# Optimization experiments

Hardware: AMD Instinct MI355X
Metric: run time of the kernel (lower is better)

## Reference

```python
import jax, jax.numpy as jnp
import numpy as np

N_NODES = 40000
N_EDGES = 640000
D = 128


def setup_inputs() -> dict:
    key = jax.random.key(0)
    ks = jax.random.split(key, 7)
    x = jax.random.normal(ks[0], (N_NODES, D), dtype=jnp.float32)
    edge_index = jax.random.randint(ks[1], (2, N_EDGES), 0, N_NODES, dtype=jnp.int64)
    # uniform in [0.5, 1.5) to avoid division blow-up near zero
    edge_attr = jax.random.uniform(ks[2], (N_EDGES,), dtype=jnp.float32) + 0.5
    s = 1.0 / np.sqrt(D)
    W1 = jax.random.uniform(ks[3], (D, D), dtype=jnp.float32, minval=-s, maxval=s)
    b1 = jax.random.uniform(ks[4], (D,), dtype=jnp.float32, minval=-s, maxval=s)
    W2 = jax.random.uniform(ks[5], (D, D), dtype=jnp.float32, minval=-s, maxval=s)
    b2 = jax.random.uniform(ks[6], (D,), dtype=jnp.float32, minval=-s, maxval=s)
    return {"x": x, "edge_index": edge_index, "edge_attr": edge_attr,
            "W1": W1, "b1": b1, "W2": W2, "b2": b2}


def _layer(x, src, dst, edge_attr, W, b, num_nodes):
    # message: gather source features, divide by per-edge scalar
    msg = x[src] / edge_attr[:, None]                      # [E, D]
    # aggregate: scatter-add into destination nodes
    agg = jax.ops.segment_sum(msg, dst, num_segments=num_nodes)  # [N, D]
    # linear (torch: y = x @ W.T + b) then leaky_relu(0.01)
    y = agg @ W.T + b
    return jnp.where(y >= 0, y, 0.01 * y)


def reference(x, edge_index, edge_attr, W1, b1, W2, b2):
    src, dst = edge_index[0], edge_index[1]
    n = x.shape[0]
    x = jnp.maximum(_layer(x, src, dst, edge_attr, W1, b1, n), 0.0)
    x = jnp.maximum(_layer(x, src, dst, edge_attr, W2, b2, n), 0.0)
    return x
```

## Files before the change

### kernel.cpp

```cpp
#include <hip/hip_runtime.h>

#define D 128
#define CAP 64
typedef unsigned short u16;
typedef unsigned int   u32;

typedef __attribute__((ext_vector_type(8))) short short8;
typedef __attribute__((ext_vector_type(4))) float f32x4;

__device__ __forceinline__ u32 f2bf(float f) {
    u32 u = __float_as_uint(f);
    u += 0x7fffu + ((u >> 16) & 1u);
    return u >> 16;
}
__device__ __forceinline__ float2 bf2x2(u32 u) {
    float2 r;
    r.x = __uint_as_float(u << 16);
    r.y = __uint_as_float(u & 0xffff0000u);
    return r;
}

__global__ __launch_bounds__(256) void prep_kernel(
    const float4* __restrict__ x, uint2* __restrict__ xb,
    const float4* __restrict__ W1, const float4* __restrict__ W2,
    uint2* __restrict__ wb1, uint2* __restrict__ wb2,
    const int* __restrict__ src, const int* __restrict__ dst,
    const float* __restrict__ attr, int* __restrict__ counts,
    u32* __restrict__ combo, int E, int n4, int cvtb)
{
    const int bid = blockIdx.x;
    const int t   = threadIdx.x;

    if (bid < cvtb) {
        int i = bid * 256 + t;
        if (i < n4) {
            float4 v = x[i];
            uint2 o;
            o.x = f2bf(v.x) | (f2bf(v.y) << 16);
            o.y = f2bf(v.z) | (f2bf(v.w) << 16);
            xb[i] = o;
        }
    } else if (bid < cvtb + 32) {
        int i = (bid - cvtb) * 256 + t;
        const float4* in = (i < 4096) ? W1 : W2;
        uint2* out = (i < 4096) ? wb1 : wb2;
        int k = i & 4095;
        float4 v = in[k];
        uint2 o;
        o.x = f2bf(v.x) | (f2bf(v.y) << 16);
        o.y = f2bf(v.z) | (f2bf(v.w) << 16);
        out[k] = o;
    } else {
        long long e0 = (long long)(bid - cvtb - 32) * 1024 + t * 4;
        if (e0 + 3 < E) {
            int4   s4 = *(const int4*)(src + e0);
            int4   d4 = *(const int4*)(dst + e0);
            float4 a4 = *(const float4*)(attr + e0);
            int r0 = atomicAdd(&counts[d4.x], 1);
            int r1 = atomicAdd(&counts[d4.y], 1);
            int r2 = atomicAdd(&counts[d4.z], 1);
            int r3 = atomicAdd(&counts[d4.w], 1);
            if (r0 < CAP) combo[((long long)d4.x << 6) + r0] = (u32)s4.x | (f2bf(1.0f / a4.x) << 16);
            if (r1 < CAP) combo[((long long)d4.y << 6) + r1] = (u32)s4.y | (f2bf(1.0f / a4.y) << 16);
            if (r2 < CAP) combo[((long long)d4.z << 6) + r2] = (u32)s4.z | (f2bf(1.0f / a4.z) << 16);
            if (r3 < CAP) combo[((long long)d4.w << 6) + r3] = (u32)s4.w | (f2bf(1.0f / a4.w) << 16);
        } else {
            for (int q = 0; q < 4; ++q) {
                long long e = e0 + q;
                if (e < E) {
                    int dd = dst[e];
                    int r = atomicAdd(&counts[dd], 1);
                    if (r < CAP)
                        combo[((long long)dd << 6) + r] =
                            (u32)src[e] | (f2bf(1.0f / attr[e]) << 16);
                }
            }
        }
    }
}

__global__ __launch_bounds__(256) void gather_kernel(
    const u16* __restrict__ x, const u32* __restrict__ combo,
    const int* __restrict__ counts, u16* __restrict__ agg, int N)
{
    const int node = (blockIdx.x * 256 + threadIdx.x) >> 6;
    if (node >= N) return;
    const int lane = threadIdx.x & 63;

    const int cnt = min(counts[node], CAP);
    const u32 ce = combo[((long long)node << 6) + lane];

    float2 acc[8];
    #pragma unroll
    for (int q = 0; q < 8; ++q) acc[q] = {0.f, 0.f};

    int j = 0;
    for (; j + 7 < cnt; j += 8) {
        u32 ed[8], rw[8];
        #pragma unroll
        for (int q = 0; q < 8; ++q) ed[q] = __shfl(ce, j + q);
        #pragma unroll
        for (int q = 0; q < 8; ++q)
            rw[q] = *(const u32*)(x + (long long)(ed[q] & 0xffffu) * D + lane * 2);
        #pragma unroll
        for (int q = 0; q < 8; ++q) {
            float f = __uint_as_float(ed[q] & 0xffff0000u);
            float2 v = bf2x2(rw[q]);
            acc[q].x += v.x * f; acc[q].y += v.y * f;
        }
    }
    for (; j + 3 < cnt; j += 4) {
        u32 ed[4], rw[4];
        #pragma unroll
        for (int q = 0; q < 4; ++q) ed[q] = __shfl(ce, j + q);
        #pragma unroll
        for (int q = 0; q < 4; ++q)
            rw[q] = *(const u32*)(x + (long long)(ed[q] & 0xffffu) * D + lane * 2);
        #pragma unroll
        for (int q = 0; q < 4; ++q) {
            float f = __uint_as_float(ed[q] & 0xffff0000u);
            float2 v = bf2x2(rw[q]);
            acc[q].x += v.x * f; acc[q].y += v.y * f;
        }
    }
    for (; j < cnt; ++j) {
        u32 e = __shfl(ce, j);
        u32 r = *(const u32*)(x + (long long)(e & 0xffffu) * D + lane * 2);
        float f = __uint_as_float(e & 0xffff0000u);
        float2 v = bf2x2(r);
        acc[0].x += v.x * f; acc[0].y += v.y * f;
    }

    float s0 = ((acc[0].x + acc[1].x) + (acc[2].x + acc[3].x))
             + ((acc[4].x + acc[5].x) + (acc[6].x + acc[7].x));
    float s1 = ((acc[0].y + acc[1].y) + (acc[2].y + acc[3].y))
             + ((acc[4].y + acc[5].y) + (acc[6].y + acc[7].y));
    u32 o = f2bf(s0) | (f2bf(s1) << 16);
    *(u32*)(agg + (long long)node * D + lane * 2) = o;
}

template <bool OUT_BF16>
__global__ __launch_bounds__(256) void mfma_gemm_kernel(
    const u16* __restrict__ A, const u16* __restrict__ Wb,
    const float* __restrict__ b, void* __restrict__ Yv, int N)
{
    const int wv   = threadIdx.x >> 6;
    const int lane = threadIdx.x & 63;
    const int m0   = (blockIdx.x * 4 + wv) * 16;
    const int mrow = lane & 15;
    const int kq   = lane >> 4;

    const u16* arow = A + (long long)(m0 + mrow) * D + kq * 8;
    short8 afr[4];
    #pragma unroll
    for (int ks = 0; ks < 4; ++ks)
        afr[ks] = *(const short8*)(arow + ks * 32);

    #pragma unroll 1
    for (int j = 0; j < 8; ++j) {
        float bias = b[j * 16 + mrow];
        f32x4 acc = {bias, bias, bias, bias};
        const u16* wrow = Wb + (long long)(j * 16 + mrow) * D + kq * 8;
        #pragma unroll
        for (int ks = 0; ks < 4; ++ks) {
            short8 bfr = *(const short8*)(wrow + ks * 32);
            acc = __builtin_amdgcn_mfma_f32_16x16x32_bf16(afr[ks], bfr, acc, 0, 0, 0);
        }
        #pragma unroll
        for (int r = 0; r < 4; ++r) {
            float v = acc[r] > 0.f ? acc[r] : 0.f;
            int row = m0 + kq * 4 + r;
            int col = j * 16 + mrow;
            if (OUT_BF16)
                *((u16*)Yv + (long long)row * D + col) = (u16)f2bf(v);
            else
                *((float*)Yv + (long long)row * D + col) = v;
        }
    }
}

extern "C" void kernel_launch(void* const* d_in, const int* in_sizes, int n_in,
                              void* d_out, int out_size, void* d_ws, size_t ws_size,
                              hipStream_t stream)
{
    const float* x    = (const float*)d_in[0];
    const int*   eidx = (const int*)d_in[1];
    const float* attr = (const float*)d_in[2];
    const float* W1   = (const float*)d_in[3];
    const float* b1   = (const float*)d_in[4];
    const float* W2   = (const float*)d_in[5];
    const float* b2   = (const float*)d_in[6];

    const int N = in_sizes[0] / D;
    const int E = in_sizes[2];
    const int* src = eidx;
    const int* dst = eidx + E;

    char* p = (char*)d_ws;
    u16*  xb    = (u16*)p;   p += ((size_t)N * D * 2 + 15) & ~15ULL;
    u16*  aggB  = (u16*)p;   p += ((size_t)N * D * 2 + 15) & ~15ULL;
    u32*  combo = (u32*)p;   p += (size_t)N * CAP * 4;
    u16*  wb1   = (u16*)p;   p += (size_t)D * D * 2;
    u16*  wb2   = (u16*)p;   p += (size_t)D * D * 2;
    int*  counts= (int*)p;

    const int n4    = N * D / 4;
    const int cvtb  = (n4 + 255) / 256;
    const int hfb   = (E + 1023) / 1024;
    const int prepb = cvtb + 32 + hfb;
    const int gatherb = (N + 3) / 4;
    const int gemmb   = (N + 63) / 64;

    hipMemsetAsync(counts, 0, (size_t)N * 4, stream);
    prep_kernel<<<prepb, 256, 0, stream>>>(
        (const float4*)x, (uint2*)xb, (const float4*)W1, (const float4*)W2,
        (uint2*)wb1, (uint2*)wb2, src, dst, attr, counts,
        combo, E, n4, cvtb);

    gather_kernel<<<gatherb, 256, 0, stream>>>(xb, combo, counts, aggB, N);
    mfma_gemm_kernel<true><<<gemmb, 256, 0, stream>>>(aggB, wb1, b1, aggB, N);

    gather_kernel<<<gatherb, 256, 0, stream>>>(aggB, combo, counts, xb, N);
    mfma_gemm_kernel<false><<<gemmb, 256, 0, stream>>>(xb, wb2, b2, d_out, N);
}
```

Measured before the change: 198.9 us.

## Partition edge bucketing and gather by XCD to localize atomics and L2 traffic

The edge-bucketing phase is launched 8 times wider. Each block filters edges so that it only handles destinations in the node range owned by its XCD, assigned round-robin by block index, which keeps the counts atomics and combo writes inside one L2. The gather kernel remaps blocks so that each XCD processes a contiguous slice of nodes, and that slice matches the one used when the combo buckets were built. The cost is that every edge is read 8 times, and the layout relies on blocks being dispatched round-robin across 8 XCDs.

```diff
diff --git a/kernel.cpp b/kernel.cpp
--- a/kernel.cpp
+++ b/kernel.cpp
@@ -26,7 +26,7 @@
     uint2* __restrict__ wb1, uint2* __restrict__ wb2,
     const int* __restrict__ src, const int* __restrict__ dst,
     const float* __restrict__ attr, int* __restrict__ counts,
-    u32* __restrict__ combo, int E, int n4, int cvtb)
+    u32* __restrict__ combo, int E, int n4, int cvtb, int Nper, int N)
 {
     const int bid = blockIdx.x;
     const int t   = threadIdx.x;
@@ -51,28 +51,40 @@
         o.y = f2bf(v.z) | (f2bf(v.w) << 16);
         out[k] = o;
     } else {
-        long long e0 = (long long)(bid - cvtb - 32) * 1024 + t * 4;
+        const int sb    = bid - cvtb - 32;
+        const int xcd   = sb & 7;
+        const int chunk = sb >> 3;
+        const int lo    = xcd * Nper;
+        const int hi    = min(lo + Nper, N);
+        long long e0 = (long long)chunk * 1024 + t * 4;
+
         if (e0 + 3 < E) {
             int4   s4 = *(const int4*)(src + e0);
             int4   d4 = *(const int4*)(dst + e0);
             float4 a4 = *(const float4*)(attr + e0);
-            int r0 = atomicAdd(&counts[d4.x], 1);
-            int r1 = atomicAdd(&counts[d4.y], 1);
-            int r2 = atomicAdd(&counts[d4.z], 1);
-            int r3 = atomicAdd(&counts[d4.w], 1);
-            if (r0 < CAP) combo[((long long)d4.x << 6) + r0] = (u32)s4.x | (f2bf(1.0f / a4.x) << 16);
-            if (r1 < CAP) combo[((long long)d4.y << 6) + r1] = (u32)s4.y | (f2bf(1.0f / a4.y) << 16);
-            if (r2 < CAP) combo[((long long)d4.z << 6) + r2] = (u32)s4.z | (f2bf(1.0f / a4.z) << 16);
-            if (r3 < CAP) combo[((long long)d4.w << 6) + r3] = (u32)s4.w | (f2bf(1.0f / a4.w) << 16);
+            #pragma unroll
+            for (int q = 0; q < 4; ++q) {
+                int d = (q == 0) ? d4.x : (q == 1) ? d4.y : (q == 2) ? d4.z : d4.w;
+                if (d >= lo && d < hi) {
+                    int s = (q == 0) ? s4.x : (q == 1) ? s4.y : (q == 2) ? s4.z : s4.w;
+                    float a = (q == 0) ? a4.x : (q == 1) ? a4.y : (q == 2) ? a4.z : a4.w;
+                    int r = atomicAdd(&counts[d], 1);
+                    if (r < CAP)
+                        combo[((long long)d << 6) + r] =
+                            (u32)s | (f2bf(1.0f / a) << 16);
+                }
+            }
         } else {
             for (int q = 0; q < 4; ++q) {
                 long long e = e0 + q;
                 if (e < E) {
-                    int dd = dst[e];
-                    int r = atomicAdd(&counts[dd], 1);
-                    if (r < CAP)
-                        combo[((long long)dd << 6) + r] =
-                            (u32)src[e] | (f2bf(1.0f / attr[e]) << 16);
+                    int d = dst[e];
+                    if (d >= lo && d < hi) {
+                        int r = atomicAdd(&counts[d], 1);
+                        if (r < CAP)
+                            combo[((long long)d << 6) + r] =
+                                (u32)src[e] | (f2bf(1.0f / attr[e]) << 16);
+                    }
                 }
             }
         }
@@ -81,10 +93,12 @@
 
 __global__ __launch_bounds__(256) void gather_kernel(
     const u16* __restrict__ x, const u32* __restrict__ combo,
-    const int* __restrict__ counts, u16* __restrict__ agg, int N)
-{
-    const int node = (blockIdx.x * 256 + threadIdx.x) >> 6;
-    if (node >= N) return;
+    const int* __restrict__ counts, u16* __restrict__ agg, int Nper, int N)
+{
+    const int xcd   = blockIdx.x & 7;
+    const int slice = blockIdx.x >> 3;
+    const int node  = xcd * Nper + slice * 4 + (threadIdx.x >> 6);
+    if (node >= N || (slice * 4 + (threadIdx.x >> 6)) >= Nper) return;
     const int lane = threadIdx.x & 63;
 
     const int cnt = min(counts[node], CAP);
@@ -195,6 +209,7 @@
     const int E = in_sizes[2];
     const int* src = eidx;
     const int* dst = eidx + E;
+    const int Nper = (N + 7) / 8;
 
     char* p = (char*)d_ws;
     u16*  xb    = (u16*)p;   p += ((size_t)N * D * 2 + 15) & ~15ULL;
@@ -206,20 +221,20 @@
 
     const int n4    = N * D / 4;
     const int cvtb  = (n4 + 255) / 256;
-    const int hfb   = (E + 1023) / 1024;
+    const int hfb   = 8 * ((E + 1023) / 1024);
     const int prepb = cvtb + 32 + hfb;
-    const int gatherb = (N + 3) / 4;
+    const int gatherb = 8 * ((Nper + 3) / 4);
     const int gemmb   = (N + 63) / 64;
 
     hipMemsetAsync(counts, 0, (size_t)N * 4, stream);
     prep_kernel<<<prepb, 256, 0, stream>>>(
         (const float4*)x, (uint2*)xb, (const float4*)W1, (const float4*)W2,
         (uint2*)wb1, (uint2*)wb2, src, dst, attr, counts,
-        combo, E, n4, cvtb);
-
-    gather_kernel<<<gatherb, 256, 0, stream>>>(xb, combo, counts, aggB, N);
+        combo, E, n4, cvtb, Nper, N);
+
+    gather_kernel<<<gatherb, 256, 0, stream>>>(xb, combo, counts, aggB, Nper, N);
     mfma_gemm_kernel<true><<<gemmb, 256, 0, stream>>>(aggB, wb1, b1, aggB, N);
 
-    gather_kernel<<<gatherb, 256, 0, stream>>>(aggB, combo, counts, xb, N);
+    gather_kernel<<<gatherb, 256, 0, stream>>>(aggB, combo, counts, xb, Nper, N);
     mfma_gemm_kernel<false><<<gemmb, 256, 0, stream>>>(xb, wb2, b2, d_out, N);
 }
```

Result: faster. 194.7 us (-2.1%).
